# Performance work log

Measured on AMD Instinct MI355X. Metric: run time of the kernel, lower is better.

## Reference

```python
import jax, jax.numpy as jnp
import numpy as np
import math

EPS = 1e-5
ANGLES = [0, 30, 45, 60, 90, 135]
SIGMA = 0.3
POOL = 7  # top-hat neighbourhood


def make_masks(H, W):
    # Soft Gaussian stripe masks, one per angle: [A, H, W]
    ys = np.linspace(-1.0, 1.0, H)
    xs = np.linspace(-1.0, 1.0, W)
    gy, gx = np.meshgrid(ys, xs, indexing='ij')
    ms = []
    for a in ANGLES:
        t = a * math.pi / 180.0
        perp = gx * (-math.sin(t)) + gy * math.cos(t)
        ms.append(np.exp(-0.5 * (perp / SIGMA) ** 2))
    return jnp.asarray(np.stack(ms, axis=0), dtype=jnp.float32)


def dwconv1d(x, w):
    # x: [B, C, L], w: [C, 1, K] depthwise, 'same' padding (odd K)
    return jax.lax.conv_general_dilated(
        x, w, window_strides=(1,), padding='SAME',
        feature_group_count=x.shape[1],
        dimension_numbers=('NCH', 'OIH', 'NCH'))


def bn(x, gamma, beta, axes, pshape):
    # Training-mode batch norm (biased variance, as in torch forward)
    mean = x.mean(axes, keepdims=True)
    var = x.var(axes, keepdims=True)
    return (x - mean) * jax.lax.rsqrt(var + EPS) * gamma.reshape(pshape) + beta.reshape(pshape)


def maxpool_same(x, k):
    # torch MaxPool2d(k, stride=1, padding=k//2): pad with -inf
    p = k // 2
    return jax.lax.reduce_window(
        x, -jnp.inf, jax.lax.max,
        window_dimensions=(1, 1, k, k), window_strides=(1, 1, 1, 1),
        padding=[(0, 0), (0, 0), (p, p), (p, p)])


def setup_inputs() -> dict:
    key = jax.random.key(0)
    ks = jax.random.split(key, 8)
    B, C, H, W = 128, 576, 28, 28
    K = 3
    x = jax.random.normal(ks[0], (B, C, H, W), dtype=jnp.float32)
    h_w = jax.random.normal(ks[1], (C, 1, K), dtype=jnp.float32) * 0.2
    v_w = jax.random.normal(ks[2], (C, 1, K), dtype=jnp.float32) * 0.2
    f_w = jax.random.normal(ks[3], (C,), dtype=jnp.float32) * 0.2  # 1x1 dw conv = per-channel scale
    h_g = jnp.ones((C,), jnp.float32); h_b = jnp.zeros((C,), jnp.float32)
    v_g = jnp.ones((C,), jnp.float32); v_b = jnp.zeros((C,), jnp.float32)
    f_g = jnp.ones((C,), jnp.float32); f_b = jnp.zeros((C,), jnp.float32)
    return {"x": x, "h_w": h_w, "h_g": h_g, "h_b": h_b,
            "v_w": v_w, "v_g": v_g, "v_b": v_b,
            "f_w": f_w, "f_g": f_g, "f_b": f_b}


def reference(x, h_w, h_g, h_b, v_w, v_g, v_b, f_w, f_g, f_b):
    B, C, H, W = x.shape
    # Horizontal stream: mean over W -> dw conv1d over H -> BN1d -> sigmoid -> [B,C,H,1]
    ph = x.mean(axis=-1)                                   # [B, C, H]
    A_h = jax.nn.sigmoid(bn(dwconv1d(ph, h_w), h_g, h_b, (0, 2), (1, C, 1)))[..., None]
    # Vertical stream: mean over H -> dw conv1d over W -> BN1d -> sigmoid -> [B,C,1,W]
    pv = x.mean(axis=-2)                                   # [B, C, W]
    A_v = jax.nn.sigmoid(bn(dwconv1d(pv, v_w), v_g, v_b, (0, 2), (1, C, 1)))[:, :, None, :]
    # Focal spot stream: white top-hat -> per-channel scale -> BN2d -> sigmoid
    spots = maxpool_same(x, POOL) - x                      # [B, C, H, W]
    A_f = jax.nn.sigmoid(bn(spots * f_w[None, :, None, None], f_g, f_b, (0, 2, 3), (1, C, 1, 1)))
    # Orientation bank: masked global means, sigmoid per angle, mean over angles
    masks = make_masks(H, W)                               # [A, H, W]
    resp = jnp.einsum('bchw,ahw->bca', x, masks) / (H * W) # [B, C, A]
    A_t = jax.nn.sigmoid(resp).mean(axis=-1)[:, :, None, None]
    return x * A_h * A_v * A_f * A_t
```

## Files before the change

### kernel.cpp

```cpp
#include <hip/hip_runtime.h>
#include <math.h>

#define B 128
#define C 576
#define H 28
#define W 28
#define HW 784
#define NPLANE (B * C)
#define RMROWS 34

typedef float nfloat4 __attribute__((ext_vector_type(4)));

__device__ __forceinline__ float sigm(float z) { return 1.f / (1.f + __expf(-z)); }

__device__ __forceinline__ float4 fmax4(float4 a, float4 b) {
    a.x = fmaxf(a.x, b.x); a.y = fmaxf(a.y, b.y);
    a.z = fmaxf(a.z, b.z); a.w = fmaxf(a.w, b.w);
    return a;
}

__device__ __forceinline__ float4 hmax13(float4 Mv, float4 Lv, float4 Rv) {
    float mm   = fmaxf(fmaxf(Mv.x, Mv.y), fmaxf(Mv.z, Mv.w));
    float l23  = fmaxf(Lv.z, Lv.w);
    float l123 = fmaxf(Lv.y, l23);
    float r01  = fmaxf(Rv.x, Rv.y);
    float r012 = fmaxf(r01, Rv.z);
    float4 o;
    o.x = fmaxf(l123, mm);
    o.y = fmaxf(l23, fmaxf(mm, Rv.x));
    o.z = fmaxf(Lv.w, fmaxf(mm, r01));
    o.w = fmaxf(mm, r012);
    return o;
}

__device__ __forceinline__ float dpp_sum64(float v) {
    int t;
    t = __builtin_amdgcn_update_dpp(0, __float_as_int(v), 0x111, 0xf, 0xf, true);  v += __int_as_float(t);
    t = __builtin_amdgcn_update_dpp(0, __float_as_int(v), 0x112, 0xf, 0xf, true);  v += __int_as_float(t);
    t = __builtin_amdgcn_update_dpp(0, __float_as_int(v), 0x114, 0xf, 0xf, true);  v += __int_as_float(t);
    t = __builtin_amdgcn_update_dpp(0, __float_as_int(v), 0x118, 0xf, 0xf, true);  v += __int_as_float(t);
    t = __builtin_amdgcn_update_dpp(0, __float_as_int(v), 0x142, 0xa, 0xf, false); v += __int_as_float(t);
    t = __builtin_amdgcn_update_dpp(0, __float_as_int(v), 0x143, 0xc, 0xf, false); v += __int_as_float(t);
    return v;
}

__device__ __forceinline__ float rl63(float v) {
    return __int_as_float(__builtin_amdgcn_readlane(__float_as_int(v), 63));
}

__device__ __forceinline__ void wave_lds_fence() {
    asm volatile("s_waitcnt lgkmcnt(0)" ::: "memory");
    __builtin_amdgcn_sched_barrier(0);
}

__global__ void k0_init(float* __restrict__ masks, float* __restrict__ acc) {
    int idx = blockIdx.x * 256 + threadIdx.x;
    if (idx < 6 * C) acc[idx] = 0.f;
    if (idx < 6 * HW) {
        int a = idx / HW;
        int p = idx - a * HW;
        int r = p / W;
        int col = p - r * W;
        const float degs[6] = {0.f, 30.f, 45.f, 60.f, 90.f, 135.f};
        float t = degs[a] * 0.017453292519943295f;
        float gy = -1.f + r * (2.f / 27.f);
        float gx = -1.f + col * (2.f / 27.f);
        float perp = gx * (-sinf(t)) + gy * cosf(t);
        float z = perp * (1.f / 0.3f);
        masks[idx] = expf(-0.5f * z * z);
    }
}

__global__ __launch_bounds__(256, 7) void k1_stats(
    const float* __restrict__ x,
    const float* __restrict__ h_w, const float* __restrict__ v_w,
    const float* __restrict__ f_w,
    float* __restrict__ yh, float* __restrict__ yv,
    float* __restrict__ acc)
{
    const int tid = threadIdx.x;
    const int wvi = __builtin_amdgcn_readfirstlane(tid >> 6);
    const int l   = tid & 63;
    const int plane = blockIdx.x * 4 + wvi;
    const int c = plane % C;
    const float* xp = x + (size_t)plane * HW;

    __shared__ __align__(16) float uA[4][RMROWS * W];
    __shared__ __align__(16) float cpA[4][196];
    __shared__ __align__(16) float rpA[4][196];
    float* rm  = uA[wvi];
    float* sxv = rm + 3 * W;
    float* cp  = cpA[wvi];
    float* rp  = rpA[wvi];

    const int r0 = l / 7;
    const int u  = l - r0 * 7;
    const int q  = u * 4;
    const int qL = u ? q - 4 : 0;
    const int qR = (u < 6) ? q + 4 : 24;
    const bool act = (l < 49);

    float4 Mv[4];
    float fs = 0.f, fss = 0.f;

    if (act) {
        float4 ca = make_float4(0.f, 0.f, 0.f, 0.f);
        float rw0, rw1, rw2, rw3;
        #pragma unroll
        for (int k = 0; k < 4; ++k) {
            const int unit = l + 49 * k;
            float4 v = ((const float4*)xp)[unit];
            Mv[k] = v;
            ((float4*)sxv)[unit] = v;
            ca.x += v.x; ca.y += v.y; ca.z += v.z; ca.w += v.w;
            float rs = (v.x + v.y) + (v.z + v.w);
            if (k == 0) rw0 = rs; else if (k == 1) rw1 = rs;
            else if (k == 2) rw2 = rs; else rw3 = rs;
        }
        ((float4*)cp)[l] = ca;
        ((float4*)rp)[l] = make_float4(rw0, rw1, rw2, rw3);
    }
    wave_lds_fence();

    if (act) {
        #pragma unroll
        for (int k = 0; k < 4; ++k) {
            const int r = r0 + 7 * k;
            const float* row = sxv + r * W;
            float4 Lv = *(const float4*)(row + qL);
            float4 Rv = *(const float4*)(row + qR);
            float4 hv = hmax13(Mv[k], Lv, Rv);
            *(float4*)(rm + (r + 3) * W + q) = hv;
            if (k == 0 && r0 == 0) {
                *(float4*)(rm + 0 * W + q) = hv;
                *(float4*)(rm + 1 * W + q) = hv;
                *(float4*)(rm + 2 * W + q) = hv;
            }
            if (k == 3 && r0 == 6) {
                *(float4*)(rm + 31 * W + q) = hv;
                *(float4*)(rm + 32 * W + q) = hv;
                *(float4*)(rm + 33 * W + q) = hv;
            }
        }
    }
    wave_lds_fence();

    const float fwc = f_w[c];
    if (act) {
        #pragma unroll
        for (int k = 0; k < 4; ++k) {
            const int r = r0 + 7 * k;
            const float* vb = rm + r * W + q;
            float4 m = *(const float4*)vb;
            m = fmax4(m, *(const float4*)(vb + W));
            m = fmax4(m, *(const float4*)(vb + 2 * W));
            m = fmax4(m, *(const float4*)(vb + 3 * W));
            m = fmax4(m, *(const float4*)(vb + 4 * W));
            m = fmax4(m, *(const float4*)(vb + 5 * W));
            m = fmax4(m, *(const float4*)(vb + 6 * W));
            float s0 = (m.x - Mv[k].x) * fwc;
            float s1 = (m.y - Mv[k].y) * fwc;
            float s2 = (m.z - Mv[k].z) * fwc;
            float s3 = (m.w - Mv[k].w) * fwc;
            fs  += (s0 + s1) + (s2 + s3);
            fss += (s0 * s0 + s1 * s1) + (s2 * s2 + s3 * s3);
        }
    }

    float ph_r = 0.f;
    float4 pvv = make_float4(0.f, 0.f, 0.f, 0.f);
    if (l < 28) {
        const int rr = l % 7, kk = l / 7;
        const float* rb = rp + rr * 28 + kk;
        float s = ((rb[0] + rb[4]) + (rb[8] + rb[12]))
                + ((rb[16] + rb[20]) + rb[24]);
        ph_r = s * (1.f / 28.f);
    }
    if (l < 7) {
        const float4* cb = (const float4*)cp;
        float4 a = cb[l];
        #pragma unroll
        for (int j = 1; j < 7; ++j) {
            float4 b = cb[l + 7 * j];
            a.x += b.x; a.y += b.y; a.z += b.z; a.w += b.w;
        }
        pvv.x = a.x * (1.f / 28.f); pvv.y = a.y * (1.f / 28.f);
        pvv.z = a.z * (1.f / 28.f); pvv.w = a.w * (1.f / 28.f);
    }

    const float hw0 = h_w[c * 3], hw1 = h_w[c * 3 + 1], hw2 = h_w[c * 3 + 2];
    float yhv = 0.f;
    {
        float pm = __shfl_up(ph_r, 1);
        float pp = __shfl_down(ph_r, 1);
        if (l < 28) {
            float a = (l > 0) ? pm : 0.f;
            float d = (l < 27) ? pp : 0.f;
            yhv = hw0 * a + hw1 * ph_r + hw2 * d;
            yh[(size_t)plane * H + l] = yhv;
        }
    }
    const float vw0 = v_w[c * 3], vw1 = v_w[c * 3 + 1], vw2 = v_w[c * 3 + 2];
    float yvs = 0.f, yvq = 0.f;
    {
        float lf = __shfl_up(pvv.w, 1);
        float rg = __shfl_down(pvv.x, 1);
        if (l < 7) {
            float a0 = (l > 0) ? lf : 0.f;
            float d3 = (l < 6) ? rg : 0.f;
            float4 y;
            y.x = vw0 * a0    + vw1 * pvv.x + vw2 * pvv.y;
            y.y = vw0 * pvv.x + vw1 * pvv.y + vw2 * pvv.z;
            y.z = vw0 * pvv.y + vw1 * pvv.z + vw2 * pvv.w;
            y.w = vw0 * pvv.z + vw1 * pvv.w + vw2 * d3;
            ((float4*)(yv + (size_t)plane * W))[l] = y;
            yvs = (y.x + y.y) + (y.z + y.w);
            yvq = (y.x * y.x + y.y * y.y) + (y.z * y.z + y.w * y.w);
        }
    }
    float yhq = yhv * yhv;

    fs = dpp_sum64(fs);  fss = dpp_sum64(fss);
    yhv = dpp_sum64(yhv); yhq = dpp_sum64(yhq);
    yvs = dpp_sum64(yvs); yvq = dpp_sum64(yvq);

    if (l == 63) {
        atomicAdd(&acc[0 * C + c], yhv);
        atomicAdd(&acc[1 * C + c], yhq);
        atomicAdd(&acc[2 * C + c], yvs);
        atomicAdd(&acc[3 * C + c], yvq);
        atomicAdd(&acc[4 * C + c], fs);
        atomicAdd(&acc[5 * C + c], fss);
    }
}

__global__ __launch_bounds__(64) void k2_params(
    const float* __restrict__ acc,
    const float* __restrict__ hg, const float* __restrict__ hb,
    const float* __restrict__ vg, const float* __restrict__ vb,
    const float* __restrict__ fg, const float* __restrict__ fb,
    float* __restrict__ params)
{
    int c = blockIdx.x * 64 + threadIdx.x;
    if (c >= C) return;
    const float inv_nh = 1.f / (float)(B * H);
    const float inv_nf = 1.f / (float)(B * HW);
    float m, v, sc;
    m = acc[c] * inv_nh;
    v = acc[C + c] * inv_nh - m * m;
    sc = hg[c] * rsqrtf(v + 1e-5f);
    params[c * 8 + 0] = sc; params[c * 8 + 1] = hb[c] - m * sc;

    m = acc[2 * C + c] * inv_nh;
    v = acc[3 * C + c] * inv_nh - m * m;
    sc = vg[c] * rsqrtf(v + 1e-5f);
    params[c * 8 + 2] = sc; params[c * 8 + 3] = vb[c] - m * sc;

    m = acc[4 * C + c] * inv_nf;
    v = acc[5 * C + c] * inv_nf - m * m;
    sc = fg[c] * rsqrtf(v + 1e-5f);
    params[c * 8 + 4] = sc; params[c * 8 + 5] = fb[c] - m * sc;
}

__global__ __launch_bounds__(256, 8) void k3_apply(
    const float* __restrict__ x, const float* __restrict__ f_w,
    const float* __restrict__ masks,
    const float* __restrict__ yh, const float* __restrict__ yv,
    const float* __restrict__ params,
    float* __restrict__ out)
{
    const int tid = threadIdx.x;
    const int wvi = __builtin_amdgcn_readfirstlane(tid >> 6);
    const int l   = tid & 63;
    const int plane = blockIdx.x * 4 + wvi;
    const int c = plane % C;
    const float* xp = x + (size_t)plane * HW;

    __shared__ __align__(16) float uA[4][RMROWS * W];
    float* rm  = uA[wvi];
    float* sxv = rm + 3 * W;

    const int r0 = l / 7;
    const int u  = l - r0 * 7;
    const int q  = u * 4;
    const int qL = u ? q - 4 : 0;
    const int qR = (u < 6) ? q + 4 : 24;
    const bool act = (l < 49);

    const float4 pA = *(const float4*)(params + c * 8);
    const float2 pB = *(const float2*)(params + c * 8 + 4);
    const float fwc = f_w[c];

    const float4* mk0 = (const float4*)(masks);
    const float4* mk1 = (const float4*)(masks + HW);
    const float4* mk2 = (const float4*)(masks + 2 * HW);
    const float4* mk3 = (const float4*)(masks + 3 * HW);
    const float4* mk4 = (const float4*)(masks + 4 * HW);
    const float4* mk5 = (const float4*)(masks + 5 * HW);

    float4 Mv[4];
    float o0=0.f,o1=0.f,o2=0.f,o3=0.f,o4=0.f,o5=0.f;

    if (act) {
        #pragma unroll
        for (int k = 0; k < 4; ++k) {
            const int unit = l + 49 * k;
            float4 v = ((const float4*)xp)[unit];
            Mv[k] = v;
            ((float4*)sxv)[unit] = v;
            float4 m;
            m = mk0[unit]; o0 += v.x*m.x + v.y*m.y + v.z*m.z + v.w*m.w;
            m = mk1[unit]; o1 += v.x*m.x + v.y*m.y + v.z*m.z + v.w*m.w;
            m = mk2[unit]; o2 += v.x*m.x + v.y*m.y + v.z*m.z + v.w*m.w;
            m = mk3[unit]; o3 += v.x*m.x + v.y*m.y + v.z*m.z + v.w*m.w;
            m = mk4[unit]; o4 += v.x*m.x + v.y*m.y + v.z*m.z + v.w*m.w;
            m = mk5[unit]; o5 += v.x*m.x + v.y*m.y + v.z*m.z + v.w*m.w;
        }
    }
    wave_lds_fence();

    if (act) {
        #pragma unroll
        for (int k = 0; k < 4; ++k) {
            const int r = r0 + 7 * k;
            const float* row = sxv + r * W;
            float4 Lv = *(const float4*)(row + qL);
            float4 Rv = *(const float4*)(row + qR);
            float4 hv = hmax13(Mv[k], Lv, Rv);
            *(float4*)(rm + (r + 3) * W + q) = hv;
            if (k == 0 && r0 == 0) {
                *(float4*)(rm + 0 * W + q) = hv;
                *(float4*)(rm + 1 * W + q) = hv;
                *(float4*)(rm + 2 * W + q) = hv;
            }
            if (k == 3 && r0 == 6) {
                *(float4*)(rm + 31 * W + q) = hv;
                *(float4*)(rm + 32 * W + q) = hv;
                *(float4*)(rm + 33 * W + q) = hv;
            }
        }
    }
    o0 = dpp_sum64(o0); o1 = dpp_sum64(o1); o2 = dpp_sum64(o2);
    o3 = dpp_sum64(o3); o4 = dpp_sum64(o4); o5 = dpp_sum64(o5);
    const float inv784 = 1.f / (float)HW;
    float ts = sigm(rl63(o0) * inv784) + sigm(rl63(o1) * inv784)
             + sigm(rl63(o2) * inv784) + sigm(rl63(o3) * inv784)
             + sigm(rl63(o4) * inv784) + sigm(rl63(o5) * inv784);
    const float atv = ts * (1.f / 6.f);
    wave_lds_fence();

    if (act) {
        float4 yv4 = ((const float4*)(yv + (size_t)plane * W))[u];
        float4 av;
        av.x = sigm(pA.z * yv4.x + pA.w);
        av.y = sigm(pA.z * yv4.y + pA.w);
        av.z = sigm(pA.z * yv4.z + pA.w);
        av.w = sigm(pA.z * yv4.w + pA.w);
        nfloat4* op = (nfloat4*)(out + (size_t)plane * HW);
        #pragma unroll
        for (int k = 0; k < 4; ++k) {
            const int r = r0 + 7 * k;
            const float* vb = rm + r * W + q;
            float4 m = *(const float4*)vb;
            m = fmax4(m, *(const float4*)(vb + W));
            m = fmax4(m, *(const float4*)(vb + 2 * W));
            m = fmax4(m, *(const float4*)(vb + 3 * W));
            m = fmax4(m, *(const float4*)(vb + 4 * W));
            m = fmax4(m, *(const float4*)(vb + 5 * W));
            m = fmax4(m, *(const float4*)(vb + 6 * W));
            float ahk = sigm(pA.x * yh[(size_t)plane * H + r] + pA.y) * atv;
            nfloat4 o;
            o.x = Mv[k].x * ahk * av.x * sigm(pB.x * ((m.x - Mv[k].x) * fwc) + pB.y);
            o.y = Mv[k].y * ahk * av.y * sigm(pB.x * ((m.y - Mv[k].y) * fwc) + pB.y);
            o.z = Mv[k].z * ahk * av.z * sigm(pB.x * ((m.z - Mv[k].z) * fwc) + pB.y);
            o.w = Mv[k].w * ahk * av.w * sigm(pB.x * ((m.w - Mv[k].w) * fwc) + pB.y);
            __builtin_nontemporal_store(o, &op[l + 49 * k]);
        }
    }
}

extern "C" void kernel_launch(void* const* d_in, const int* in_sizes, int n_in,
                              void* d_out, int out_size, void* d_ws, size_t ws_size,
                              hipStream_t stream) {
    const float* x   = (const float*)d_in[0];
    const float* h_w = (const float*)d_in[1];
    const float* h_g = (const float*)d_in[2];
    const float* h_b = (const float*)d_in[3];
    const float* v_w = (const float*)d_in[4];
    const float* v_g = (const float*)d_in[5];
    const float* v_b = (const float*)d_in[6];
    const float* f_w = (const float*)d_in[7];
    const float* f_g = (const float*)d_in[8];
    const float* f_b = (const float*)d_in[9];
    float* out = (float*)d_out;
    float* ws = (float*)d_ws;

    float* masks  = ws;
    float* acc    = ws + 4704;
    float* params = ws + 8160;
    float* yh     = ws + 12768;
    float* yv     = ws + 2077152;

    k0_init<<<19, 256, 0, stream>>>(masks, acc);
    k1_stats<<<NPLANE / 4, 256, 0, stream>>>(x, h_w, v_w, f_w, yh, yv, acc);
    k2_params<<<9, 64, 0, stream>>>(acc, h_g, h_b, v_g, v_b, f_g, f_b, params);
    k3_apply<<<NPLANE / 4, 256, 0, stream>>>(x, f_w, masks, yh, yv, params, out);
}
```

Baseline: 200.6 us.

## Move orientation-bank mask dot products from apply kernel into stats kernel

The six masked global sums and their sigmoid average are now computed in the stats kernel while x is already loaded, and stored per plane in a new workspace array that the apply kernel reads. The per-channel focal weight is folded into the BN params, and the focal-stat scaling moves to the final atomic, which trims arithmetic in both passes. This lightens the apply kernel, which is probably on the critical path, at the cost of extra mask loads and registers in the stats kernel plus one extra small buffer.

Measured after the change: 190.3 us. 1.05x faster.

```diff
diff --git a/kernel.cpp b/kernel.cpp
--- a/kernel.cpp
+++ b/kernel.cpp
@@ -42,10 +42,6 @@
     t = __builtin_amdgcn_update_dpp(0, __float_as_int(v), 0x142, 0xa, 0xf, false); v += __int_as_float(t);
     t = __builtin_amdgcn_update_dpp(0, __float_as_int(v), 0x143, 0xc, 0xf, false); v += __int_as_float(t);
     return v;
-}
-
-__device__ __forceinline__ float rl63(float v) {
-    return __int_as_float(__builtin_amdgcn_readlane(__float_as_int(v), 63));
 }
 
 __device__ __forceinline__ void wave_lds_fence() {
@@ -74,9 +70,9 @@
 __global__ __launch_bounds__(256, 7) void k1_stats(
     const float* __restrict__ x,
     const float* __restrict__ h_w, const float* __restrict__ v_w,
-    const float* __restrict__ f_w,
+    const float* __restrict__ f_w, const float* __restrict__ masks,
     float* __restrict__ yh, float* __restrict__ yv,
-    float* __restrict__ acc)
+    float* __restrict__ at, float* __restrict__ acc)
 {
     const int tid = threadIdx.x;
     const int wvi = __builtin_amdgcn_readfirstlane(tid >> 6);
@@ -100,25 +96,50 @@
     const int qR = (u < 6) ? q + 4 : 24;
     const bool act = (l < 49);
 
+    const float4* mk0 = (const float4*)(masks);
+    const float4* mk1 = (const float4*)(masks + HW);
+    const float4* mk2 = (const float4*)(masks + 2 * HW);
+    const float4* mk3 = (const float4*)(masks + 3 * HW);
+    const float4* mk4 = (const float4*)(masks + 4 * HW);
+    const float4* mk5 = (const float4*)(masks + 5 * HW);
+
     float4 Mv[4];
     float fs = 0.f, fss = 0.f;
 
-    if (act) {
-        float4 ca = make_float4(0.f, 0.f, 0.f, 0.f);
-        float rw0, rw1, rw2, rw3;
-        #pragma unroll
-        for (int k = 0; k < 4; ++k) {
-            const int unit = l + 49 * k;
-            float4 v = ((const float4*)xp)[unit];
-            Mv[k] = v;
-            ((float4*)sxv)[unit] = v;
-            ca.x += v.x; ca.y += v.y; ca.z += v.z; ca.w += v.w;
-            float rs = (v.x + v.y) + (v.z + v.w);
-            if (k == 0) rw0 = rs; else if (k == 1) rw1 = rs;
-            else if (k == 2) rw2 = rs; else rw3 = rs;
-        }
-        ((float4*)cp)[l] = ca;
-        ((float4*)rp)[l] = make_float4(rw0, rw1, rw2, rw3);
+    {
+        float o0=0.f,o1=0.f,o2=0.f,o3=0.f,o4=0.f,o5=0.f;
+        if (act) {
+            float4 ca = make_float4(0.f, 0.f, 0.f, 0.f);
+            float rw0, rw1, rw2, rw3;
+            #pragma unroll
+            for (int k = 0; k < 4; ++k) {
+                const int unit = l + 49 * k;
+                float4 v = ((const float4*)xp)[unit];
+                Mv[k] = v;
+                ((float4*)sxv)[unit] = v;
+                ca.x += v.x; ca.y += v.y; ca.z += v.z; ca.w += v.w;
+                float rs = (v.x + v.y) + (v.z + v.w);
+                if (k == 0) rw0 = rs; else if (k == 1) rw1 = rs;
+                else if (k == 2) rw2 = rs; else rw3 = rs;
+                float4 m;
+                m = mk0[unit]; o0 += v.x*m.x + v.y*m.y + v.z*m.z + v.w*m.w;
+                m = mk1[unit]; o1 += v.x*m.x + v.y*m.y + v.z*m.z + v.w*m.w;
+                m = mk2[unit]; o2 += v.x*m.x + v.y*m.y + v.z*m.z + v.w*m.w;
+                m = mk3[unit]; o3 += v.x*m.x + v.y*m.y + v.z*m.z + v.w*m.w;
+                m = mk4[unit]; o4 += v.x*m.x + v.y*m.y + v.z*m.z + v.w*m.w;
+                m = mk5[unit]; o5 += v.x*m.x + v.y*m.y + v.z*m.z + v.w*m.w;
+            }
+            ((float4*)cp)[l] = ca;
+            ((float4*)rp)[l] = make_float4(rw0, rw1, rw2, rw3);
+        }
+        o0 = dpp_sum64(o0); o1 = dpp_sum64(o1); o2 = dpp_sum64(o2);
+        o3 = dpp_sum64(o3); o4 = dpp_sum64(o4); o5 = dpp_sum64(o5);
+        if (l == 63) {
+            const float inv784 = 1.f / (float)HW;
+            float t = sigm(o0 * inv784) + sigm(o1 * inv784) + sigm(o2 * inv784)
+                    + sigm(o3 * inv784) + sigm(o4 * inv784) + sigm(o5 * inv784);
+            at[plane] = t * (1.f / 6.f);
+        }
     }
     wave_lds_fence();
 
@@ -145,7 +166,6 @@
     }
     wave_lds_fence();
 
-    const float fwc = f_w[c];
     if (act) {
         #pragma unroll
         for (int k = 0; k < 4; ++k) {
@@ -158,10 +178,10 @@
             m = fmax4(m, *(const float4*)(vb + 4 * W));
             m = fmax4(m, *(const float4*)(vb + 5 * W));
             m = fmax4(m, *(const float4*)(vb + 6 * W));
-            float s0 = (m.x - Mv[k].x) * fwc;
-            float s1 = (m.y - Mv[k].y) * fwc;
-            float s2 = (m.z - Mv[k].z) * fwc;
-            float s3 = (m.w - Mv[k].w) * fwc;
+            float s0 = m.x - Mv[k].x;
+            float s1 = m.y - Mv[k].y;
+            float s2 = m.z - Mv[k].z;
+            float s3 = m.w - Mv[k].w;
             fs  += (s0 + s1) + (s2 + s3);
             fss += (s0 * s0 + s1 * s1) + (s2 * s2 + s3 * s3);
         }
@@ -225,17 +245,18 @@
     yvs = dpp_sum64(yvs); yvq = dpp_sum64(yvq);
 
     if (l == 63) {
+        const float fwc = f_w[c];
         atomicAdd(&acc[0 * C + c], yhv);
         atomicAdd(&acc[1 * C + c], yhq);
         atomicAdd(&acc[2 * C + c], yvs);
         atomicAdd(&acc[3 * C + c], yvq);
-        atomicAdd(&acc[4 * C + c], fs);
-        atomicAdd(&acc[5 * C + c], fss);
+        atomicAdd(&acc[4 * C + c], fs * fwc);
+        atomicAdd(&acc[5 * C + c], fss * fwc * fwc);
     }
 }
 
 __global__ __launch_bounds__(64) void k2_params(
-    const float* __restrict__ acc,
+    const float* __restrict__ acc, const float* __restrict__ f_w,
     const float* __restrict__ hg, const float* __restrict__ hb,
     const float* __restrict__ vg, const float* __restrict__ vb,
     const float* __restrict__ fg, const float* __restrict__ fb,
@@ -259,14 +280,14 @@
     m = acc[4 * C + c] * inv_nf;
     v = acc[5 * C + c] * inv_nf - m * m;
     sc = fg[c] * rsqrtf(v + 1e-5f);
-    params[c * 8 + 4] = sc; params[c * 8 + 5] = fb[c] - m * sc;
+    params[c * 8 + 4] = sc * f_w[c];
+    params[c * 8 + 5] = fb[c] - m * sc;
 }
 
 __global__ __launch_bounds__(256, 8) void k3_apply(
-    const float* __restrict__ x, const float* __restrict__ f_w,
-    const float* __restrict__ masks,
+    const float* __restrict__ x,
     const float* __restrict__ yh, const float* __restrict__ yv,
-    const float* __restrict__ params,
+    const float* __restrict__ at, const float* __restrict__ params,
     float* __restrict__ out)
 {
     const int tid = threadIdx.x;
@@ -289,32 +310,16 @@
 
     const float4 pA = *(const float4*)(params + c * 8);
     const float2 pB = *(const float2*)(params + c * 8 + 4);
-    const float fwc = f_w[c];
-
-    const float4* mk0 = (const float4*)(masks);
-    const float4* mk1 = (const float4*)(masks + HW);
-    const float4* mk2 = (const float4*)(masks + 2 * HW);
-    const float4* mk3 = (const float4*)(masks + 3 * HW);
-    const float4* mk4 = (const float4*)(masks + 4 * HW);
-    const float4* mk5 = (const float4*)(masks + 5 * HW);
+    const float atv = at[plane];
 
     float4 Mv[4];
-    float o0=0.f,o1=0.f,o2=0.f,o3=0.f,o4=0.f,o5=0.f;
 
     if (act) {
         #pragma unroll
         for (int k = 0; k < 4; ++k) {
             const int unit = l + 49 * k;
-            float4 v = ((const float4*)xp)[unit];
-            Mv[k] = v;
-            ((float4*)sxv)[unit] = v;
-            float4 m;
-            m = mk0[unit]; o0 += v.x*m.x + v.y*m.y + v.z*m.z + v.w*m.w;
-            m = mk1[unit]; o1 += v.x*m.x + v.y*m.y + v.z*m.z + v.w*m.w;
-            m = mk2[unit]; o2 += v.x*m.x + v.y*m.y + v.z*m.z + v.w*m.w;
-            m = mk3[unit]; o3 += v.x*m.x + v.y*m.y + v.z*m.z + v.w*m.w;
-            m = mk4[unit]; o4 += v.x*m.x + v.y*m.y + v.z*m.z + v.w*m.w;
-            m = mk5[unit]; o5 += v.x*m.x + v.y*m.y + v.z*m.z + v.w*m.w;
+            Mv[k] = ((const float4*)xp)[unit];
+            ((float4*)sxv)[unit] = Mv[k];
         }
     }
     wave_lds_fence();
@@ -340,13 +345,6 @@
             }
         }
     }
-    o0 = dpp_sum64(o0); o1 = dpp_sum64(o1); o2 = dpp_sum64(o2);
-    o3 = dpp_sum64(o3); o4 = dpp_sum64(o4); o5 = dpp_sum64(o5);
-    const float inv784 = 1.f / (float)HW;
-    float ts = sigm(rl63(o0) * inv784) + sigm(rl63(o1) * inv784)
-             + sigm(rl63(o2) * inv784) + sigm(rl63(o3) * inv784)
-             + sigm(rl63(o4) * inv784) + sigm(rl63(o5) * inv784);
-    const float atv = ts * (1.f / 6.f);
     wave_lds_fence();
 
     if (act) {
@@ -370,10 +368,10 @@
             m = fmax4(m, *(const float4*)(vb + 6 * W));
             float ahk = sigm(pA.x * yh[(size_t)plane * H + r] + pA.y) * atv;
             nfloat4 o;
-            o.x = Mv[k].x * ahk * av.x * sigm(pB.x * ((m.x - Mv[k].x) * fwc) + pB.y);
-            o.y = Mv[k].y * ahk * av.y * sigm(pB.x * ((m.y - Mv[k].y) * fwc) + pB.y);
-            o.z = Mv[k].z * ahk * av.z * sigm(pB.x * ((m.z - Mv[k].z) * fwc) + pB.y);
-            o.w = Mv[k].w * ahk * av.w * sigm(pB.x * ((m.w - Mv[k].w) * fwc) + pB.y);
+            o.x = Mv[k].x * ahk * av.x * sigm(fmaf(pB.x, m.x, fmaf(-pB.x, Mv[k].x, pB.y)));
+            o.y = Mv[k].y * ahk * av.y * sigm(fmaf(pB.x, m.y, fmaf(-pB.x, Mv[k].y, pB.y)));
+            o.z = Mv[k].z * ahk * av.z * sigm(fmaf(pB.x, m.z, fmaf(-pB.x, Mv[k].z, pB.y)));
+            o.w = Mv[k].w * ahk * av.w * sigm(fmaf(pB.x, m.w, fmaf(-pB.x, Mv[k].w, pB.y)));
             __builtin_nontemporal_store(o, &op[l + 49 * k]);
         }
     }
@@ -398,11 +396,12 @@
     float* masks  = ws;
     float* acc    = ws + 4704;
     float* params = ws + 8160;
-    float* yh     = ws + 12768;
-    float* yv     = ws + 2077152;
+    float* at     = ws + 12768;
+    float* yh     = ws + 86496;
+    float* yv     = ws + 2150880;
 
     k0_init<<<19, 256, 0, stream>>>(masks, acc);
-    k1_stats<<<NPLANE / 4, 256, 0, stream>>>(x, h_w, v_w, f_w, yh, yv, acc);
-    k2_params<<<9, 64, 0, stream>>>(acc, h_g, h_b, v_g, v_b, f_g, f_b, params);
-    k3_apply<<<NPLANE / 4, 256, 0, stream>>>(x, f_w, masks, yh, yv, params, out);
-}
+    k1_stats<<<NPLANE / 4, 256, 0, stream>>>(x, h_w, v_w, f_w, masks, yh, yv, at, acc);
+    k2_params<<<9, 64, 0, stream>>>(acc, f_w, h_g, h_b, v_g, v_b, f_g, f_b, params);
+    k3_apply<<<NPLANE / 4, 256, 0, stream>>>(x, yh, yv, at, params, out);
+}
```
